# Kernel optimization log

Measured on AMD Instinct MI355X. Metric: run time of the kernel, lower is better.

The kernel has to match this reference:

```python
import jax, jax.numpy as jnp
import numpy as np

N_NODES = 100000
N_EDGES = 1600000
HIDDEN = 64
N_LAYERS = 3
N_CLASSES = 2
N_GRAPHS = 128
NEG_SLOPE = 0.2  # PyG GATConv default negative_slope


def setup_inputs() -> dict:
    key = jax.random.key(0)
    ks = jax.random.split(key, 8)
    x = jax.random.randint(ks[0], (N_NODES,), 0, 2)
    edge_index = jax.random.randint(ks[1], (2, N_EDGES), 0, N_NODES)
    batch = jnp.sort(jax.random.randint(ks[2], (N_NODES,), 0, N_GRAPHS))
    scale = 1.0 / np.sqrt(HIDDEN)
    embed_table = jax.random.normal(ks[3], (2, HIDDEN), jnp.float32)
    Ws = jax.random.normal(ks[4], (N_LAYERS, HIDDEN, HIDDEN), jnp.float32) * scale
    a_srcs = jax.random.normal(ks[5], (N_LAYERS, HIDDEN), jnp.float32) * scale
    a_dsts = jax.random.normal(ks[6], (N_LAYERS, HIDDEN), jnp.float32) * scale
    biases = jnp.zeros((N_LAYERS, HIDDEN), jnp.float32)
    W_out = jax.random.normal(ks[7], (HIDDEN, N_CLASSES), jnp.float32) * scale
    b_out = jnp.zeros((N_CLASSES,), jnp.float32)
    return {"x": x, "edge_index": edge_index, "batch": batch,
            "embed_table": embed_table, "Ws": Ws, "a_srcs": a_srcs,
            "a_dsts": a_dsts, "biases": biases, "W_out": W_out, "b_out": b_out}


def _gat_layer(h, src, dst, W, a_s, a_d, b):
    # h: [N, D]; src/dst: [E'] (self loops included) -> PyG GATConv, heads=1
    hW = h @ W                                   # [N, D]
    e = jax.nn.leaky_relu((hW @ a_s)[src] + (hW @ a_d)[dst], NEG_SLOPE)  # [E']
    m = jax.ops.segment_max(e, dst, num_segments=N_NODES)               # stable softmax per dst
    ex = jnp.exp(e - m[dst])
    denom = jax.ops.segment_sum(ex, dst, num_segments=N_NODES)
    alpha = ex / denom[dst]                      # [E']
    out = jax.ops.segment_sum(hW[src] * alpha[:, None], dst, num_segments=N_NODES)
    return out + b


def reference(x, edge_index, batch, embed_table, Ws, a_srcs, a_dsts, biases, W_out, b_out):
    loop = jnp.arange(N_NODES)
    src = jnp.concatenate([edge_index[0], loop])  # PyG add_self_loops=True
    dst = jnp.concatenate([edge_index[1], loop])
    h = embed_table[x]                            # [N, D]
    for l in range(N_LAYERS):
        h = _gat_layer(h, src, dst, Ws[l], a_srcs[l], a_dsts[l], biases[l])
        if l < N_LAYERS - 1:
            h = jax.nn.relu(h)
    sums = jax.ops.segment_sum(h, batch, num_segments=N_GRAPHS)
    counts = jax.ops.segment_sum(jnp.ones((N_NODES,), h.dtype), batch, num_segments=N_GRAPHS)
    pooled = sums / jnp.maximum(counts, 1.0)[:, None]  # global_mean_pool
    return pooled @ W_out + b_out                      # [G, num_classes]
```

## Files before the change

kernel.cpp:

```cpp
#include <hip/hip_runtime.h>
#include <hip/hip_bf16.h>
#include <float.h>

#define N_NODES 100000
#define N_EDGES 1600000
#define HIDDEN 64
#define N_GRAPHS 128
#define NEG_SLOPE 0.2f
#define ETOT (N_EDGES + N_NODES)

#define BSHIFT 9
#define NB ((N_NODES + 511) >> BSHIFT)
#define PAIR_CHUNK 4096
#define PAIR_BLOCKS ((N_EDGES + PAIR_CHUNK - 1) / PAIR_CHUNK)
#define XBIT_BLOCKS ((N_NODES + 255) / 256)
#define TBL_BLOCKS (NLVL / 4)
#define CAP 12288

#define NREP 64
#define REP_STRIDE 272
#define NLVL 512

__device__ __forceinline__ unsigned short f2bf(float f) {
    unsigned u = __float_as_uint(f);
    unsigned r = (u + 0x7FFFu + ((u >> 16) & 1u)) >> 16;
    return (unsigned short)r;
}
__device__ __forceinline__ float blo(unsigned u) { return __uint_as_float(u << 16); }
__device__ __forceinline__ float bhi(unsigned u) { return __uint_as_float(u & 0xFFFF0000u); }
__device__ __forceinline__ int sb0(unsigned u) { return (int)((unsigned)(u << 24)) >> 24; }
__device__ __forceinline__ int sb1(unsigned u) { return (int)((unsigned)(u << 16)) >> 24; }
__device__ __forceinline__ int sb2(unsigned u) { return (int)((unsigned)(u << 8)) >> 24; }
__device__ __forceinline__ int sb3(unsigned u) { return (int)u >> 24; }


__global__ __launch_bounds__(256) void k_prep(
    const int* __restrict__ x,
    const float* __restrict__ embed, const float* __restrict__ Ws,
    const float* __restrict__ biases, const float* __restrict__ a_srcs,
    const float* __restrict__ a_dsts, const float* __restrict__ W_out,
    int* __restrict__ gcnt, float* __restrict__ pool_acc,
    unsigned* __restrict__ xb,
    unsigned char* __restrict__ Tq8, float* __restrict__ Tscl,
    float* __restrict__ Ts1s, float* __restrict__ Ts1d,
    float* __restrict__ sparams)
{
    int t = threadIdx.x, b = blockIdx.x;

    if (b < TBL_BLOCKS) {
        if (b == 0 && t < NB) gcnt[t] = 0;
        if (b < NREP && t < 2 * N_GRAPHS) pool_acc[b * REP_STRIDE + t] = 0.f;

        int l = b * 4 + (t >> 6);
        int f = t & 63;
        float r0 = 0.f, r1 = 0.f;
#pragma unroll 8
        for (int k = 0; k < 64; ++k) {
            float w = Ws[k * 64 + f];
            r0 = fmaf(embed[k], w, r0);
            r1 = fmaf(embed[64 + k], w, r1);
        }
        if (l == 0) {
            float as = a_srcs[f], ad = a_dsts[f];
            float t0 = r0 * as, t1 = r1 * as, t2 = r0 * ad, t3 = r1 * ad;
#pragma unroll
            for (int off = 32; off >= 1; off >>= 1) {
                t0 += __shfl_xor(t0, off); t1 += __shfl_xor(t1, off);
                t2 += __shfl_xor(t2, off); t3 += __shfl_xor(t3, off);
            }
            if (f == 0) { sparams[0] = t0; sparams[1] = t1; sparams[2] = t2; sparams[3] = t3; }
        }
        if (l == 1) {
            float b2 = biases[128 + f];
            float t4 = b2 * W_out[f * 2];
            float t5 = b2 * W_out[f * 2 + 1];
#pragma unroll
            for (int off = 32; off >= 1; off >>= 1) {
                t4 += __shfl_xor(t4, off); t5 += __shfl_xor(t5, off);
            }
            if (f == 0) { sparams[4] = t4; sparams[5] = t5; }
        }
        float c1 = (float)l * (1.f / (NLVL - 1));
        float o = fmaxf(biases[f] + r0 + c1 * (r1 - r0), 0.f);
        const float* W1 = Ws + 4096;
        float h = 0.f;
#pragma unroll 8
        for (int k = 0; k < 64; ++k) h = fmaf(__shfl(o, k), W1[k * 64 + f], h);
        float ss = h * a_srcs[64 + f];
        float sd = h * a_dsts[64 + f];
        float am = fabsf(h);
#pragma unroll
        for (int off = 32; off >= 1; off >>= 1) {
            ss += __shfl_xor(ss, off);
            sd += __shfl_xor(sd, off);
            am = fmaxf(am, __shfl_xor(am, off));
        }
        float iscl = (am > 0.f) ? 127.f / am : 0.f;
        Tq8[l * 64 + f] = (unsigned char)(__float2int_rn(h * iscl) & 255);
        if (f == 0) { Tscl[l] = am * (1.f / 127.f); Ts1s[l] = ss; Ts1d[l] = sd; }
    } else {
        int i = (b - TBL_BLOCKS) * 256 + t;
        int lane = t & 63;
        bool bb = (i < N_NODES) && (x[i] != 0);
        unsigned long long m = __ballot(bb);
        int wid = i >> 6;
        if (i < N_NODES + 64) {
            if (lane == 0) xb[wid * 2] = (unsigned)m;
            if (lane == 32) xb[wid * 2 + 1] = (unsigned)(m >> 32);
        }
    }
}


__global__ __launch_bounds__(256) void k_scatter(
    const int* __restrict__ e0, const int* __restrict__ e1,
    const unsigned* __restrict__ xb, int* __restrict__ gcnt,
    int* __restrict__ pairs)
{
    __shared__ int hcnt[NB];
    __shared__ int base[NB];
    int t = threadIdx.x, b = blockIdx.x;
    if (t < NB) hcnt[t] = 0;
    __syncthreads();
    int ebase = b * PAIR_CHUNK;
    int ecount = min(PAIR_CHUNK, N_EDGES - ebase);
    for (int i = 4 * t; i < ecount; i += 1024) {
        int4 d4 = *(const int4*)(e1 + ebase + i);
        atomicAdd(&hcnt[d4.x >> BSHIFT], 1);
        atomicAdd(&hcnt[d4.y >> BSHIFT], 1);
        atomicAdd(&hcnt[d4.z >> BSHIFT], 1);
        atomicAdd(&hcnt[d4.w >> BSHIFT], 1);
    }
    __syncthreads();
    if (t < NB) {
        int c = hcnt[t];
        base[t] = c ? atomicAdd(&gcnt[t], c) : 0;
        hcnt[t] = 0;
    }
    __syncthreads();
    for (int i = 4 * t; i < ecount; i += 1024) {
        int4 s4 = *(const int4*)(e0 + ebase + i);
        int4 d4 = *(const int4*)(e1 + ebase + i);
        int ss[4] = {s4.x, s4.y, s4.z, s4.w};
        int dd[4] = {d4.x, d4.y, d4.z, d4.w};
#pragma unroll
        for (int j = 0; j < 4; ++j) {
            int s = ss[j], d = dd[j];
            int xv = (xb[s >> 5] >> (s & 31)) & 1;
            int B = d >> BSHIFT;
            int idx = atomicAdd(&hcnt[B], 1);
            pairs[B * CAP + base[B] + idx] = (xv << 26) | ((d & 511) << 17) | s;
        }
    }
}

__global__ __launch_bounds__(1024) void k_csr_bucket(
    const int* __restrict__ pairs, const int* __restrict__ gcnt,
    const int* __restrict__ x, const float* __restrict__ sparams,
    int* __restrict__ rowptr, int* __restrict__ col,
    unsigned short* __restrict__ cidx)
{
    __shared__ int deg[512];
    __shared__ int excl[512];
    __shared__ int cnt2[512];
    __shared__ int wsum[16];
    __shared__ int p0sh;
    int b = blockIdx.x;
    int t = threadIdx.x;
    int nb = b << BSHIFT;
    int nodes = min(512, N_NODES - nb);

    int pv = (t < b) ? gcnt[t] : 0;
#pragma unroll
    for (int off = 32; off >= 1; off >>= 1) pv += __shfl_xor(pv, off);
    if ((t & 63) == 0) wsum[t >> 6] = pv;
    __syncthreads();
    if (t == 0) {
        int s = 0;
#pragma unroll
        for (int i = 0; i < 16; ++i) s += wsum[i];
        p0sh = s;
    }

    int xself = 0;
    if (t < 512) {
        xself = (t < nodes) ? (x[nb + t] & 1) : 0;
        deg[t] = (t < nodes) ? (1 | (xself << 16)) : 0;
        cnt2[t] = 1;
    }
    __syncthreads();
    int cnt = gcnt[b];
    int pbase = b * CAP;
    for (int i = t; i < cnt; i += 1024) {
        int p = pairs[pbase + i];
        atomicAdd(&deg[(p >> 17) & 511], 1 | (((p >> 26) & 1) << 16));
    }
    __syncthreads();

    int packed = (t < 512) ? deg[t] : 0;
    int val = packed & 0xFFFF;
    int kx = packed >> 16;
    if (t < nodes) {
        float ss0 = sparams[0], ss1 = sparams[1];
        float sd = xself ? sparams[3] : sparams[2];
        float e0 = ss0 + sd; e0 = (e0 >= 0.f) ? e0 : NEG_SLOPE * e0;
        float e1 = ss1 + sd; e1 = (e1 >= 0.f) ? e1 : NEG_SLOPE * e1;
        float pp0 = __expf(e0), pp1 = __expf(e1);
        float kn = (float)kx, dn = (float)(val - kx);
        float c1 = kn * pp1 / (dn * pp0 + kn * pp1);
        cidx[nb + t] = (unsigned short)__float2int_rn(c1 * (float)(NLVL - 1));
    }

    int xx = val;
#pragma unroll
    for (int off = 1; off < 64; off <<= 1) {
        int y = __shfl_up(xx, off);
        if ((t & 63) >= off) xx += y;
    }
    if ((t & 63) == 63 && t < 512) wsum[t >> 6] = xx;
    __syncthreads();
    if (t == 0) {
        int s = 0;
#pragma unroll
        for (int i = 0; i < 8; ++i) { int v = wsum[i]; wsum[i] = s; s += v; }
    }
    __syncthreads();
    int ex = xx - val + wsum[t >> 6];
    if (t < 512) excl[t] = ex;

    int p0 = p0sh;
    int colbase = p0 + nb;
    if (t < nodes) {
        rowptr[nb + t] = colbase + ex;
        col[colbase + ex] = nb + t;
    }
    if (b == NB - 1 && t == 0) rowptr[N_NODES] = ETOT;
    __syncthreads();
    for (int i = t; i < cnt; i += 1024) {
        int p = pairs[pbase + i];
        int li = (p >> 17) & 511;
        int pos = colbase + excl[li] + atomicAdd(&cnt2[li], 1);
        col[pos] = p & 0x1FFFF;
    }
}


__global__ __launch_bounds__(256) void k_agg1(
    const unsigned char* __restrict__ Tq8, const float* __restrict__ Tscl,
    const float* __restrict__ Ts1s, const float* __restrict__ Ts1d,
    const unsigned short* __restrict__ cidx, const int* __restrict__ col,
    const int* __restrict__ rowptr, const float* __restrict__ bias,
    unsigned short* __restrict__ hout)
{
    __shared__ float2 stash[4][64];
    int t = threadIdx.x;
    int wave = t >> 6, lane = t & 63;
    int h = lane >> 5, hl = lane & 31;
    int base = blockIdx.x * 8 + wave * 2;
    if (base >= N_NODES) return;
    const char* hb = (const char*)Tq8;

    int node = base + h;
    bool valid = (node < N_NODES);
    int row = 0, end = 0;
    if (valid) { row = rowptr[node]; end = rowptr[node + 1]; }
    int deg = end - row;
    int degO = __shfl_xor(deg, 32);
    bool fast = (deg <= 32) && (degO <= 32);

    if (fast) {
        int idx = 0;
        float p = 0.f, sc = 0.f;
        if (hl < deg) idx = cidx[col[row + hl]];
        float sdi = Ts1d[__shfl(idx, h * 32)];
        if (hl < deg) {
            float ee = Ts1s[idx] + sdi;
            ee = (ee >= 0.f) ? ee : NEG_SLOPE * ee;
            p = __expf(ee);
            sc = Tscl[idx];
        }
        stash[wave][lane] = make_float2(p * sc, __int_as_float(idx * 64));

        int q = hl >> 4;
        int f = hl & 15;
        int f4 = f * 4;
        int sb = h * 32;
        float a0 = 0.f, a1 = 0.f, a2 = 0.f, a3 = 0.f;
        int degr = (deg + 7) & ~7;
        for (int j = q; j < degr; j += 8) {
            float2 e0 = stash[wave][sb + j];
            float2 e1 = stash[wave][sb + j + 2];
            float2 e2 = stash[wave][sb + j + 4];
            float2 e3 = stash[wave][sb + j + 6];
            unsigned v0 = *(const unsigned*)(hb + (__float_as_int(e0.y) + f4));
            unsigned v1 = *(const unsigned*)(hb + (__float_as_int(e1.y) + f4));
            unsigned v2 = *(const unsigned*)(hb + (__float_as_int(e2.y) + f4));
            unsigned v3 = *(const unsigned*)(hb + (__float_as_int(e3.y) + f4));
            a0 = fmaf(e0.x, (float)sb0(v0), a0);
            a1 = fmaf(e0.x, (float)sb1(v0), a1);
            a2 = fmaf(e0.x, (float)sb2(v0), a2);
            a3 = fmaf(e0.x, (float)sb3(v0), a3);
            a0 = fmaf(e1.x, (float)sb0(v1), a0);
            a1 = fmaf(e1.x, (float)sb1(v1), a1);
            a2 = fmaf(e1.x, (float)sb2(v1), a2);
            a3 = fmaf(e1.x, (float)sb3(v1), a3);
            a0 = fmaf(e2.x, (float)sb0(v2), a0);
            a1 = fmaf(e2.x, (float)sb1(v2), a1);
            a2 = fmaf(e2.x, (float)sb2(v2), a2);
            a3 = fmaf(e2.x, (float)sb3(v2), a3);
            a0 = fmaf(e3.x, (float)sb0(v3), a0);
            a1 = fmaf(e3.x, (float)sb1(v3), a1);
            a2 = fmaf(e3.x, (float)sb2(v3), a2);
            a3 = fmaf(e3.x, (float)sb3(v3), a3);
        }
        float denom = p;
#pragma unroll
        for (int off = 16; off >= 1; off >>= 1) denom += __shfl_xor(denom, off);
        float inv = 1.f / denom;
        a0 += __shfl_xor(a0, 16);
        a1 += __shfl_xor(a1, 16);
        a2 += __shfl_xor(a2, 16);
        a3 += __shfl_xor(a3, 16);
        if (hl < 16 && valid) {
            float4 bb = *(const float4*)&bias[4 * f];
            ushort4 pk;
            pk.x = f2bf(fmaxf(fmaf(a0, inv, bb.x), 0.f));
            pk.y = f2bf(fmaxf(fmaf(a1, inv, bb.y), 0.f));
            pk.z = f2bf(fmaxf(fmaf(a2, inv, bb.z), 0.f));
            pk.w = f2bf(fmaxf(fmaf(a3, inv, bb.w), 0.f));
            *(ushort4*)&hout[node * 64 + 4 * f] = pk;
        }
    } else {
        for (int s = 0; s < 2; ++s) {
            int nd = base + s;
            if (nd >= N_NODES) continue;
            int r = rowptr[nd], e = rowptr[nd + 1];
            float sdi = Ts1d[cidx[nd]];
            float m = -FLT_MAX;
            for (int j = r + lane; j < e; j += 64) {
                float ee = Ts1s[cidx[col[j]]] + sdi;
                ee = (ee >= 0.f) ? ee : NEG_SLOPE * ee;
                m = fmaxf(m, ee);
            }
#pragma unroll
            for (int off = 32; off >= 1; off >>= 1) m = fmaxf(m, __shfl_xor(m, off));
            float denom = 0.f;
            for (int j = r + lane; j < e; j += 64) {
                float ee = Ts1s[cidx[col[j]]] + sdi;
                ee = (ee >= 0.f) ? ee : NEG_SLOPE * ee;
                denom += __expf(ee - m);
            }
#pragma unroll
            for (int off = 32; off >= 1; off >>= 1) denom += __shfl_xor(denom, off);
            float inv = 1.f / denom;
            float acc = 0.f;
            for (int j = r; j < e; ++j) {
                int idxj = cidx[col[j]];
                float ee = Ts1s[idxj] + sdi;
                ee = (ee >= 0.f) ? ee : NEG_SLOPE * ee;
                float w = __expf(ee - m) * inv * Tscl[idxj];
                int bq = (int)(signed char)Tq8[idxj * 64 + lane];
                acc = fmaf(w, (float)bq, acc);
            }
            hout[nd * 64 + lane] = f2bf(fmaxf(acc + bias[lane], 0.f));
        }
    }
}


__global__ __launch_bounds__(256) void k_gemm2(
    const unsigned* __restrict__ h32, const float* __restrict__ W,
    const float* __restrict__ a_s, const float* __restrict__ a_d,
    const float* __restrict__ W_out,
    float2* __restrict__ z2, float* __restrict__ s_src, float* __restrict__ s_dst)
{
    __shared__ float Wl[64 * 64];
    __shared__ float hT[64 * 68];
    int t = threadIdx.x;
    int r0 = blockIdx.x * 64;

    for (int i = t; i < 4096; i += 256) Wl[i] = W[i];
    for (int i = t; i < 2048; i += 256) {
        int r = i >> 5, m = i & 31;
        int row = r0 + r;
        unsigned u = (row < N_NODES) ? h32[row * 32 + m] : 0u;
        hT[(2 * m) * 68 + r]     = blo(u);
        hT[(2 * m + 1) * 68 + r] = bhi(u);
    }
    __syncthreads();

    int tcol = t & 15;
    int trow = t >> 4;
    float acc[4][4];
#pragma unroll
    for (int i = 0; i < 4; ++i)
#pragma unroll
        for (int j = 0; j < 4; ++j) acc[i][j] = 0.f;

    for (int k = 0; k < 64; ++k) {
        float4 va = *(const float4*)&hT[k * 68 + trow * 4];
        float4 vb = *(const float4*)&Wl[k * 64 + tcol * 4];
        float a[4] = {va.x, va.y, va.z, va.w};
        float bb[4] = {vb.x, vb.y, vb.z, vb.w};
#pragma unroll
        for (int i = 0; i < 4; ++i)
#pragma unroll
            for (int j = 0; j < 4; ++j) acc[i][j] = fmaf(a[i], bb[j], acc[i][j]);
    }

    float4 as4 = *(const float4*)&a_s[tcol * 4];
    float4 ad4 = *(const float4*)&a_d[tcol * 4];
    float asr[4] = {as4.x, as4.y, as4.z, as4.w};
    float adr[4] = {ad4.x, ad4.y, ad4.z, ad4.w};
    float4 wa = *(const float4*)&W_out[8 * tcol];
    float4 wb = *(const float4*)&W_out[8 * tcol + 4];

#pragma unroll
    for (int i = 0; i < 4; ++i) {
        int row = r0 + trow * 4 + i;
        float ps = 0.f, pd = 0.f;
#pragma unroll
        for (int j = 0; j < 4; ++j) {
            ps = fmaf(acc[i][j], asr[j], ps);
            pd = fmaf(acc[i][j], adr[j], pd);
        }
        float z0 = acc[i][0] * wa.x + acc[i][1] * wa.z + acc[i][2] * wb.x + acc[i][3] * wb.z;
        float z1 = acc[i][0] * wa.y + acc[i][1] * wa.w + acc[i][2] * wb.y + acc[i][3] * wb.w;
#pragma unroll
        for (int off = 8; off >= 1; off >>= 1) {
            ps += __shfl_xor(ps, off);
            pd += __shfl_xor(pd, off);
            z0 += __shfl_xor(z0, off);
            z1 += __shfl_xor(z1, off);
        }
        if (row < N_NODES && tcol == 0) {
            s_src[row] = ps; s_dst[row] = pd;
            z2[row] = make_float2(z0, z1);
        }
    }
}


__global__ __launch_bounds__(256) void k_pool2(
    const float2* __restrict__ z2, const int* __restrict__ col,
    const int* __restrict__ rowptr, const float* __restrict__ s_src_in,
    const float* __restrict__ s_dst_in, const int* __restrict__ batch,
    float* __restrict__ pool_acc)
{
    int t = threadIdx.x;
    int wave = t >> 6, lane = t & 63;
    int h = lane >> 5, hl = lane & 31;
    int base0 = blockIdx.x * 32 + wave * 8;
    if (base0 >= N_NODES) return;
    float* rep = pool_acc + ((blockIdx.x * 4 + wave) & (NREP - 1)) * REP_STRIDE;

    int gcur = -1;
    float acc0 = 0.f, acc1 = 0.f;

#pragma unroll
    for (int i = 0; i < 4; ++i) {
        int node = base0 + 2 * i + h;
        bool valid = (node < N_NODES);
        int row = 0, end = 0;
        if (valid) { row = rowptr[node]; end = rowptr[node + 1]; }
        int deg = end - row;
        int degO = __shfl_xor(deg, 32);
        bool fast = (deg <= 32) && (degO <= 32);
        float r0 = 0.f, r1 = 0.f;

        if (fast) {
            float sdi = valid ? s_dst_in[node] : 0.f;
            float p = 0.f;
            float2 zv = make_float2(0.f, 0.f);
            if (hl < deg) {
                int c = col[row + hl];
                float ee = s_src_in[c] + sdi;
                ee = (ee >= 0.f) ? ee : NEG_SLOPE * ee;
                p = __expf(ee);
                zv = z2[c];
            }
            float n0 = p * zv.x, n1 = p * zv.y, dn = p;
#pragma unroll
            for (int off = 16; off >= 1; off >>= 1) {
                n0 += __shfl_xor(n0, off);
                n1 += __shfl_xor(n1, off);
                dn += __shfl_xor(dn, off);
            }
            float inv = 1.f / dn;
            r0 = n0 * inv; r1 = n1 * inv;
        } else {
            float rr0[2], rr1[2];
#pragma unroll
            for (int s = 0; s < 2; ++s) {
                rr0[s] = rr1[s] = 0.f;
                int nd = base0 + 2 * i + s;
                if (nd >= N_NODES) continue;
                int r = rowptr[nd], e = rowptr[nd + 1];
                float sdi = s_dst_in[nd];
                float n0 = 0.f, n1 = 0.f, dn = 0.f;
                for (int j = r + lane; j < e; j += 64) {
                    int c = col[j];
                    float ee = s_src_in[c] + sdi;
                    ee = (ee >= 0.f) ? ee : NEG_SLOPE * ee;
                    float p = __expf(ee);
                    float2 zv = z2[c];
                    n0 = fmaf(p, zv.x, n0);
                    n1 = fmaf(p, zv.y, n1);
                    dn += p;
                }
#pragma unroll
                for (int off = 32; off >= 1; off >>= 1) {
                    n0 += __shfl_xor(n0, off);
                    n1 += __shfl_xor(n1, off);
                    dn += __shfl_xor(dn, off);
                }
                float inv = 1.f / dn;
                rr0[s] = n0 * inv; rr1[s] = n1 * inv;
            }
            r0 = rr0[h]; r1 = rr1[h];
        }

        if (hl == 0 && valid) {
            int g = batch[node];
            if (g != gcur) {
                if (gcur >= 0) {
                    atomicAdd(&rep[gcur * 2], acc0);
                    atomicAdd(&rep[gcur * 2 + 1], acc1);
                }
                gcur = g; acc0 = r0; acc1 = r1;
            } else {
                acc0 += r0; acc1 += r1;
            }
        }
    }
    if (hl == 0 && gcur >= 0) {
        atomicAdd(&rep[gcur * 2], acc0);
        atomicAdd(&rep[gcur * 2 + 1], acc1);
    }
}


__device__ __forceinline__ int lower_bound_dev(const int* __restrict__ a, int n, int v) {
    int lo = 0, hi = n;
    while (lo < hi) {
        int mid = (lo + hi) >> 1;
        if (a[mid] < v) lo = mid + 1; else hi = mid;
    }
    return lo;
}

__global__ void k_head(const float* __restrict__ pool_acc,
                       const int* __restrict__ batch,
                       const float* __restrict__ b_out,
                       const float* __restrict__ sparams,
                       float* __restrict__ out)
{
    int t = threadIdx.x;
    if (t < 2 * N_GRAPHS) {
        float s = 0.f;
#pragma unroll 8
        for (int r = 0; r < NREP; ++r) s += pool_acc[r * REP_STRIDE + t];
        int g = t >> 1, c = t & 1;
        int start = lower_bound_dev(batch, N_NODES, g);
        int end = lower_bound_dev(batch, N_NODES, g + 1);
        float cnt = fmaxf((float)(end - start), 1.f);
        out[t] = s / cnt + sparams[4 + c] + b_out[c];
    }
}


extern "C" void kernel_launch(void* const* d_in, const int* in_sizes, int n_in,
                              void* d_out, int out_size, void* d_ws, size_t ws_size,
                              hipStream_t stream) {
    const int*   x       = (const int*)d_in[0];
    const int*   edge    = (const int*)d_in[1];
    const int*   batch   = (const int*)d_in[2];
    const float* embed   = (const float*)d_in[3];
    const float* Ws      = (const float*)d_in[4];
    const float* a_srcs  = (const float*)d_in[5];
    const float* a_dsts  = (const float*)d_in[6];
    const float* biases  = (const float*)d_in[7];
    const float* W_out   = (const float*)d_in[8];
    const float* b_out   = (const float*)d_in[9];
    float* out = (float*)d_out;

    char* ws = (char*)d_ws;
    size_t off = 0;
    auto alloc = [&](size_t bytes) -> void* {
        void* p = ws + off;
        off += (bytes + 255) & ~(size_t)255;
        return p;
    };
    unsigned short* hout  = (unsigned short*)alloc((size_t)N_NODES * 64 * sizeof(unsigned short));
    float2* z2      = (float2*)alloc((size_t)N_NODES * sizeof(float2));
    float* s_src0   = (float*)alloc((size_t)N_NODES * sizeof(float));
    float* s_dst0   = (float*)alloc((size_t)N_NODES * sizeof(float));
    unsigned short* cidx = (unsigned short*)alloc((size_t)N_NODES * sizeof(unsigned short));
    int*   rowptr   = (int*)alloc((size_t)(N_NODES + 1) * sizeof(int));
    int*   colA     = (int*)alloc((size_t)ETOT * sizeof(int));
    int*   gcnt     = (int*)alloc((size_t)NB * sizeof(int));
    float* pool_acc = (float*)alloc((size_t)(NREP * REP_STRIDE) * sizeof(float));
    unsigned* xb    = (unsigned*)alloc((size_t)3232 * sizeof(unsigned));
    unsigned char* Tq8 = (unsigned char*)alloc((size_t)NLVL * 64);
    float* Tscl     = (float*)alloc((size_t)NLVL * sizeof(float));
    float* Ts1s     = (float*)alloc((size_t)NLVL * sizeof(float));
    float* Ts1d     = (float*)alloc((size_t)NLVL * sizeof(float));
    float* sparams  = (float*)alloc((size_t)8 * sizeof(float));
    int*   pairs    = (int*)alloc((size_t)NB * CAP * sizeof(int));

    const int* e0 = edge;
    const int* e1 = edge + N_EDGES;

    k_prep<<<TBL_BLOCKS + XBIT_BLOCKS, 256, 0, stream>>>(
        x, embed, Ws, biases, a_srcs, a_dsts, W_out,
        gcnt, pool_acc, xb, Tq8, Tscl, Ts1s, Ts1d, sparams);
    k_scatter<<<PAIR_BLOCKS, 256, 0, stream>>>(e0, e1, xb, gcnt, pairs);
    k_csr_bucket<<<NB, 1024, 0, stream>>>(pairs, gcnt, x, sparams, rowptr, colA, cidx);

    k_agg1<<<(N_NODES + 7) / 8, 256, 0, stream>>>(
        Tq8, Tscl, Ts1s, Ts1d, cidx, colA, rowptr, biases + 64, hout);
    k_gemm2<<<(N_NODES + 63) / 64, 256, 0, stream>>>(
        (const unsigned*)hout, Ws + 8192, a_srcs + 128, a_dsts + 128, W_out,
        z2, s_src0, s_dst0);
    k_pool2<<<(N_NODES + 31) / 32, 256, 0, stream>>>(
        z2, colA, rowptr, s_src0, s_dst0, batch, pool_acc);
    k_head<<<1, 256, 0, stream>>>(pool_acc, batch, b_out, sparams, out);
}
```

Baseline: 211.6 us.

## Stage scatter writes in LDS, pack per-node scores into float4, cache rowptr

k_scatter now runs a block-wide prefix sum over the bucket counts, stages each pair and its destination in shared memory, and then writes them out in bucket-contiguous order, aiming for better-coalesced global stores. k_gemm2 packs s_src, z0, z1 and s_dst into one float4 per node, so the gather in k_pool2 fetches a single 16-byte record per neighbor instead of two separate random loads. k_pool2 also loads the block's rowptr slice into shared memory once. The cost is more LDS use in k_scatter (about 32 KB plus extra barriers for the scan), which can lower occupancy, and the float4 layout reads s_dst bytes that the gather does not need.

```diff
diff --git a/kernel.cpp b/kernel.cpp
--- a/kernel.cpp
+++ b/kernel.cpp
@@ -119,6 +119,10 @@
 {
     __shared__ int hcnt[NB];
     __shared__ int base[NB];
+    __shared__ int lstart[NB];
+    __shared__ int tot[256];
+    __shared__ int staged[PAIR_CHUNK];
+    __shared__ int sdest[PAIR_CHUNK];
     int t = threadIdx.x, b = blockIdx.x;
     if (t < NB) hcnt[t] = 0;
     __syncthreads();
@@ -132,9 +136,18 @@
         atomicAdd(&hcnt[d4.w >> BSHIFT], 1);
     }
     __syncthreads();
+    int v = (t < NB) ? hcnt[t] : 0;
+    tot[t] = v;
+    __syncthreads();
+    for (int off = 1; off < 256; off <<= 1) {
+        int u = (t >= off) ? tot[t - off] : 0;
+        __syncthreads();
+        tot[t] += u;
+        __syncthreads();
+    }
     if (t < NB) {
-        int c = hcnt[t];
-        base[t] = c ? atomicAdd(&gcnt[t], c) : 0;
+        lstart[t] = tot[t] - v;
+        base[t] = v ? atomicAdd(&gcnt[t], v) : 0;
         hcnt[t] = 0;
     }
     __syncthreads();
@@ -149,9 +162,14 @@
             int xv = (xb[s >> 5] >> (s & 31)) & 1;
             int B = d >> BSHIFT;
             int idx = atomicAdd(&hcnt[B], 1);
-            pairs[B * CAP + base[B] + idx] = (xv << 26) | ((d & 511) << 17) | s;
-        }
-    }
+            int lp = lstart[B] + idx;
+            staged[lp] = (xv << 26) | ((d & 511) << 17) | s;
+            sdest[lp] = B * CAP + base[B] + idx;
+        }
+    }
+    __syncthreads();
+    for (int i = t; i < ecount; i += 256)
+        pairs[sdest[i]] = staged[i];
 }
 
 __global__ __launch_bounds__(1024) void k_csr_bucket(
@@ -372,7 +390,7 @@
     const unsigned* __restrict__ h32, const float* __restrict__ W,
     const float* __restrict__ a_s, const float* __restrict__ a_d,
     const float* __restrict__ W_out,
-    float2* __restrict__ z2, float* __restrict__ s_src, float* __restrict__ s_dst)
+    float4* __restrict__ szz)
 {
     __shared__ float Wl[64 * 64];
     __shared__ float hT[64 * 68];
@@ -434,24 +452,27 @@
             z1 += __shfl_xor(z1, off);
         }
         if (row < N_NODES && tcol == 0) {
-            s_src[row] = ps; s_dst[row] = pd;
-            z2[row] = make_float2(z0, z1);
+            szz[row] = make_float4(ps, z0, z1, pd);
         }
     }
 }
 
 
 __global__ __launch_bounds__(256) void k_pool2(
-    const float2* __restrict__ z2, const int* __restrict__ col,
-    const int* __restrict__ rowptr, const float* __restrict__ s_src_in,
-    const float* __restrict__ s_dst_in, const int* __restrict__ batch,
+    const float4* __restrict__ szz, const int* __restrict__ col,
+    const int* __restrict__ rowptr, const int* __restrict__ batch,
     float* __restrict__ pool_acc)
 {
+    __shared__ int rp2[33];
     int t = threadIdx.x;
     int wave = t >> 6, lane = t & 63;
     int h = lane >> 5, hl = lane & 31;
-    int base0 = blockIdx.x * 32 + wave * 8;
-    if (base0 >= N_NODES) return;
+    int nb0 = blockIdx.x * 32;
+    if (t < 33) {
+        int n = nb0 + t;
+        rp2[t] = (n <= N_NODES) ? rowptr[n] : ETOT;
+    }
+    __syncthreads();
     float* rep = pool_acc + ((blockIdx.x * 4 + wave) & (NREP - 1)) * REP_STRIDE;
 
     int gcur = -1;
@@ -459,27 +480,28 @@
 
 #pragma unroll
     for (int i = 0; i < 4; ++i) {
-        int node = base0 + 2 * i + h;
+        int nls = wave * 8 + 2 * i + h;
+        int node = nb0 + nls;
         bool valid = (node < N_NODES);
-        int row = 0, end = 0;
-        if (valid) { row = rowptr[node]; end = rowptr[node + 1]; }
+        int row = valid ? rp2[nls] : 0;
+        int end = valid ? rp2[nls + 1] : 0;
         int deg = end - row;
         int degO = __shfl_xor(deg, 32);
         bool fast = (deg <= 32) && (degO <= 32);
         float r0 = 0.f, r1 = 0.f;
 
         if (fast) {
-            float sdi = valid ? s_dst_in[node] : 0.f;
-            float p = 0.f;
-            float2 zv = make_float2(0.f, 0.f);
+            float sdi = valid ? szz[node].w : 0.f;
+            float p = 0.f, zy = 0.f, zz = 0.f;
             if (hl < deg) {
                 int c = col[row + hl];
-                float ee = s_src_in[c] + sdi;
+                float4 sz = szz[c];
+                float ee = sz.x + sdi;
                 ee = (ee >= 0.f) ? ee : NEG_SLOPE * ee;
                 p = __expf(ee);
-                zv = z2[c];
-            }
-            float n0 = p * zv.x, n1 = p * zv.y, dn = p;
+                zy = sz.y; zz = sz.z;
+            }
+            float n0 = p * zy, n1 = p * zz, dn = p;
 #pragma unroll
             for (int off = 16; off >= 1; off >>= 1) {
                 n0 += __shfl_xor(n0, off);
@@ -493,19 +515,20 @@
 #pragma unroll
             for (int s = 0; s < 2; ++s) {
                 rr0[s] = rr1[s] = 0.f;
-                int nd = base0 + 2 * i + s;
+                int nds = wave * 8 + 2 * i + s;
+                int nd = nb0 + nds;
                 if (nd >= N_NODES) continue;
-                int r = rowptr[nd], e = rowptr[nd + 1];
-                float sdi = s_dst_in[nd];
+                int r = rp2[nds], e = rp2[nds + 1];
+                float sdi = szz[nd].w;
                 float n0 = 0.f, n1 = 0.f, dn = 0.f;
                 for (int j = r + lane; j < e; j += 64) {
                     int c = col[j];
-                    float ee = s_src_in[c] + sdi;
+                    float4 sz = szz[c];
+                    float ee = sz.x + sdi;
                     ee = (ee >= 0.f) ? ee : NEG_SLOPE * ee;
                     float p = __expf(ee);
-                    float2 zv = z2[c];
-                    n0 = fmaf(p, zv.x, n0);
-                    n1 = fmaf(p, zv.y, n1);
+                    n0 = fmaf(p, sz.y, n0);
+                    n1 = fmaf(p, sz.z, n1);
                     dn += p;
                 }
 #pragma unroll
@@ -592,9 +615,7 @@
         return p;
     };
     unsigned short* hout  = (unsigned short*)alloc((size_t)N_NODES * 64 * sizeof(unsigned short));
-    float2* z2      = (float2*)alloc((size_t)N_NODES * sizeof(float2));
-    float* s_src0   = (float*)alloc((size_t)N_NODES * sizeof(float));
-    float* s_dst0   = (float*)alloc((size_t)N_NODES * sizeof(float));
+    float4* szz     = (float4*)alloc((size_t)N_NODES * sizeof(float4));
     unsigned short* cidx = (unsigned short*)alloc((size_t)N_NODES * sizeof(unsigned short));
     int*   rowptr   = (int*)alloc((size_t)(N_NODES + 1) * sizeof(int));
     int*   colA     = (int*)alloc((size_t)ETOT * sizeof(int));
@@ -620,9 +641,8 @@
     k_agg1<<<(N_NODES + 7) / 8, 256, 0, stream>>>(
         Tq8, Tscl, Ts1s, Ts1d, cidx, colA, rowptr, biases + 64, hout);
     k_gemm2<<<(N_NODES + 63) / 64, 256, 0, stream>>>(
-        (const unsigned*)hout, Ws + 8192, a_srcs + 128, a_dsts + 128, W_out,
-        z2, s_src0, s_dst0);
+        (const unsigned*)hout, Ws + 8192, a_srcs + 128, a_dsts + 128, W_out, szz);
     k_pool2<<<(N_NODES + 31) / 32, 256, 0, stream>>>(
-        z2, colA, rowptr, s_src0, s_dst0, batch, pool_acc);
+        szz, colA, rowptr, batch, pool_acc);
     k_head<<<1, 256, 0, stream>>>(pool_acc, batch, b_out, sparams, out);
 }
```

After: 203.3 us. -3.9%, faster.
